# Kernel optimization log

Measured on AMD Instinct MI355X. Metric: run time of the kernel, lower is better.

The kernel has to match this reference:

```python
import jax, jax.numpy as jnp
import numpy as np

B, T, H = 2048, 200, 128
A0, A1 = 64, 16


def setup_inputs() -> dict:
    key = jax.random.key(0)
    ks = jax.random.split(key, 12)
    s = 0.05  # init scale (upstream uses tiny init_std; larger keeps dynamics non-trivial)
    d = {}
    d["query"] = jax.random.normal(ks[0], (B, 1, H), jnp.float32)
    d["keys"] = jax.random.normal(ks[1], (B, T, H), jnp.float32)
    d["W0"] = jax.random.normal(ks[2], (A0, 4 * H), jnp.float32) * s
    d["b0"] = jnp.zeros((A0,), jnp.float32)
    d["W1"] = jax.random.normal(ks[3], (A1, A0), jnp.float32) * s
    d["b1"] = jnp.zeros((A1,), jnp.float32)
    d["Wd"] = jax.random.normal(ks[4], (1, A1), jnp.float32) * s
    d["bd"] = jnp.zeros((1,), jnp.float32)
    d["Wih"] = jax.random.normal(ks[5], (3 * H, H), jnp.float32) * s
    d["Whh"] = jax.random.normal(ks[6], (3 * H, H), jnp.float32) * s
    d["bih"] = jnp.zeros((3 * H,), jnp.float32)
    d["bhh"] = jnp.zeros((3 * H,), jnp.float32)
    d["keys_length"] = jax.random.randint(ks[7], (B, 1), 1, T + 1, jnp.int32)
    return d


def _forward(query, keys, W0, b0, W1, b1, Wd, bd, Wih, Whh, bih, bhh, keys_length):
    b, t, h = keys.shape
    q = jnp.broadcast_to(query, (b, t, h))
    # DIN attention: concat [q, k, q-k, q*k] -> sigmoid MLP -> scalar score
    ai = jnp.concatenate([q, keys, q - keys, q * keys], axis=-1)  # [B,T,4H]
    a = jax.nn.sigmoid(jnp.einsum('bti,oi->bto', ai, W0) + b0)
    a = jax.nn.sigmoid(jnp.einsum('bti,oi->bto', a, W1) + b1)
    score = (jnp.einsum('bti,oi->bto', a, Wd) + bd)[..., 0]  # [B,T]
    valid = jnp.arange(t)[None, :] < keys_length  # [B,T] True at valid steps
    att = jnp.where(valid, score, 0.0)
    # AUGRU over packed (equiv. length-masked) sequence
    gi = jnp.einsum('bti,oi->bto', keys, Wih) + bih  # precomputed input transform [B,T,3H]

    def step(hprev, inp):
        gi_t, a_t, v_t = inp  # [B,3H], [B], [B]
        gh = hprev @ Whh.T + bhh
        i_r, i_z, i_n = jnp.split(gi_t, 3, axis=-1)
        h_r, h_z, h_n = jnp.split(gh, 3, axis=-1)
        r = jax.nn.sigmoid(i_r + h_r)
        z = jax.nn.sigmoid(i_z + h_z)
        n = jnp.tanh(i_n + r * h_n)
        z = a_t[:, None] * z  # attention-modulated update gate
        hnew = (1.0 - z) * hprev + z * n
        hnew = jnp.where(v_t[:, None], hnew, hprev)  # freeze past sequence end
        return hnew, None

    h0 = jnp.zeros((b, h), keys.dtype)
    hT, _ = jax.lax.scan(step, h0, (gi.transpose(1, 0, 2), att.T, valid.T))
    # rows with keys_length == 0 would be zero (here lengths >= 1)
    return hT * (keys_length > 0).astype(hT.dtype)


def reference(query, keys, W0, b0, W1, b1, Wd, bd, Wih, Whh, bih, bhh, keys_length):
    return _forward(query, keys, W0, b0, W1, b1, Wd, bd, Wih, Whh, bih, bhh, keys_length)
```

## Files before the change

### kernel.cpp

```cpp
#include <hip/hip_runtime.h>
#include <stdint.h>
#include <stddef.h>

#define B_N   2048
#define T_SEQ 200
#define H_DIM 128

typedef __attribute__((ext_vector_type(8))) short short8;
typedef __attribute__((ext_vector_type(4))) float floatx4;

#define OFF_ATT 0u
#define OFF_C   819200u
#define OFF_U1  1343488u
#define OFF_FR  1376256u
#define OFF_W1F 1409024u

__device__ __forceinline__ unsigned rnd_bf(float f) {
  union { float f; unsigned u; } v; v.f = f;
  return v.u + 0x7FFFu + ((v.u >> 16) & 1u);
}
__device__ __forceinline__ unsigned short f2bf(float f) {
  return (unsigned short)(rnd_bf(f) >> 16);
}
__device__ __forceinline__ unsigned pack2bf(float lo, float hi) {
  return __builtin_amdgcn_perm(rnd_bf(hi), rnd_bf(lo), 0x07060302u);
}
__device__ __forceinline__ float bf2f(unsigned short u) {
  union { unsigned u; float f; } v; v.u = ((unsigned)u) << 16; return v.f;
}

#define LOG2E 1.4426950408889634f
__device__ __forceinline__ float fsig(float x) {
  return __builtin_amdgcn_rcpf(1.0f + __builtin_amdgcn_exp2f(-LOG2E * x));
}

__device__ __forceinline__ floatx4 mfma16(short8 a, short8 b, floatx4 c) {
  return __builtin_amdgcn_mfma_f32_16x16x32_bf16(a, b, c, 0, 0, 0);
}
__device__ __forceinline__ short8 pack8s(const float* p, float s) {
  short8 r;
#pragma unroll
  for (int j = 0; j < 8; ++j) r[j] = (short)f2bf(p[j] * s);
  return r;
}

__global__ __launch_bounds__(256) void prep_kernel(
    const float* __restrict__ W0, const float* __restrict__ W1,
    float* __restrict__ u1_ws, short8* __restrict__ fr_ws,
    short8* __restrict__ w1f_ws)
{
  const int gid = blockIdx.x * 256 + threadIdx.x;
  const int gs  = gridDim.x * 256;
  for (int i = gid; i < 128 * 64; i += gs) {
    int k = i >> 6, o = i & 63;
    u1_ws[i] = W0[o * 512 + k] + W0[o * 512 + 256 + k];
  }
  for (int f = gid; f < 4 * 8 * 64; f += gs) {
    int ln = f & 63, kc = (f >> 6) & 7, tt = f >> 9;
    int o = tt * 16 + (ln & 15);
    int k0 = kc * 32 + ((ln >> 4) * 8);
    short8 v;
#pragma unroll
    for (int j = 0; j < 8; ++j) {
      int ks = k0 + j;
      float x = (ks < 128) ? (W0[o * 512 + 128 + ks] - W0[o * 512 + 256 + ks])
                           : W0[o * 512 + 384 + (ks - 128)];
      v[j] = (short)f2bf(x);
    }
    fr_ws[f] = v;
  }
  for (int f = gid; f < 2 * 64; f += gs) {
    int ln = f & 63, kc = f >> 6;
    int n = ln & 15, k0 = kc * 32 + ((ln >> 4) * 8);
    short8 v;
#pragma unroll
    for (int j = 0; j < 8; ++j) v[j] = (short)f2bf(W1[n * 64 + k0 + j]);
    w1f_ws[f] = v;
  }
}

__global__ __launch_bounds__(256) void c_kernel(
    const float* __restrict__ query, const float* __restrict__ u1_ws,
    const float* __restrict__ b0, float* __restrict__ c_ws)
{
  const int blk = blockIdx.x, tid = threadIdx.x;
  __shared__ float qs[16 * 128];
  for (int i = tid; i < 512; i += 256)
    *(float4*)&qs[i * 4] = *(const float4*)(query + (size_t)blk * 2048 + i * 4);
  __syncthreads();
  const int o = tid & 63, bb = tid >> 6;
  float a0 = b0[o], a1 = a0, a2 = a0, a3 = a0;
  const float* qr = qs + bb * 512;
#pragma unroll 4
  for (int k = 0; k < 128; ++k) {
    float w = u1_ws[k * 64 + o];
    a0 = fmaf(qr[k], w, a0);
    a1 = fmaf(qr[128 + k], w, a1);
    a2 = fmaf(qr[256 + k], w, a2);
    a3 = fmaf(qr[384 + k], w, a3);
  }
  const int b = blk * 16 + bb * 4;
  c_ws[(b + 0) * 64 + o] = a0;
  c_ws[(b + 1) * 64 + o] = a1;
  c_ws[(b + 2) * 64 + o] = a2;
  c_ws[(b + 3) * 64 + o] = a3;
}

__global__ __launch_bounds__(256) void att_kernel(
    const float* __restrict__ query, const float* __restrict__ keys,
    const float* __restrict__ c_ws, const short8* __restrict__ fr_ws,
    const short8* __restrict__ w1f_ws, const float* __restrict__ b1,
    const float* __restrict__ Wd, const float* __restrict__ bd,
    const int* __restrict__ klen, unsigned short* __restrict__ attb)
{
  const int b   = blockIdx.x;
  const int tid = threadIdx.x;
  const int lane = tid & 63, wv = tid >> 6;
  const int kb = (lane >> 4) * 8;

  __shared__ float qs[H_DIM];
  __shared__ __align__(16) unsigned short A[64][264];
  __shared__ __align__(16) unsigned short a0b[64][72];
  __shared__ float a1s[64][20];

  const int len = klen[b];

  if (tid < H_DIM) qs[tid] = query[(size_t)b * H_DIM + tid];

  short8 bf[8];
  {
    const short8* frp = fr_ws + (size_t)wv * 8 * 64;
#pragma unroll
    for (int kc = 0; kc < 8; ++kc) bf[kc] = frp[kc * 64 + lane];
  }
  short8 w1f0 = w1f_ws[lane], w1f1 = w1f_ws[64 + lane];
  const float b1v = b1[lane & 15];
  const float co = c_ws[(size_t)b * 64 + wv * 16 + (lane & 15)];
  const float bd0 = bd[0];
  float wd_r[16];
#pragma unroll
  for (int i = 0; i < 16; ++i) wd_r[i] = Wd[i];
  __syncthreads();

  int t0 = 0;
  for (; t0 < len; t0 += 64) {
    {
      int tl = tid >> 2, q4 = tid & 3;
      int tg = t0 + tl;
      bool v = (tg < T_SEQ);
      const float* krow = keys + ((size_t)b * T_SEQ + (v ? tg : 0)) * H_DIM + q4 * 32;
#pragma unroll
      for (int i = 0; i < 32; i += 4) {
        float4 kv = v ? *(const float4*)(krow + i) : make_float4(0.f, 0.f, 0.f, 0.f);
        int col = q4 * 32 + i;
        *(unsigned*)&A[tl][col]     = pack2bf(kv.x, kv.y);
        *(unsigned*)&A[tl][col + 2] = pack2bf(kv.z, kv.w);
        *(unsigned*)&A[tl][128 + col]     = pack2bf(kv.x * qs[col + 0], kv.y * qs[col + 1]);
        *(unsigned*)&A[tl][128 + col + 2] = pack2bf(kv.z * qs[col + 2], kv.w * qs[col + 3]);
      }
    }
    __syncthreads();

#pragma unroll
    for (int tt = 0; tt < 4; ++tt) {
      floatx4 acc = {co, co, co, co};
      int row = tt * 16 + (lane & 15);
#pragma unroll
      for (int kc = 0; kc < 8; ++kc)
        acc = mfma16(*(const short8*)&A[row][kc * 32 + kb], bf[kc], acc);
#pragma unroll
      for (int r = 0; r < 4; ++r)
        a0b[tt * 16 + (lane >> 4) * 4 + r][wv * 16 + (lane & 15)] = f2bf(fsig(acc[r]));
    }
    __syncthreads();

    {
      floatx4 acc1 = {b1v, b1v, b1v, b1v};
      int r2 = wv * 16 + (lane & 15);
      acc1 = mfma16(*(const short8*)&a0b[r2][kb],      w1f0, acc1);
      acc1 = mfma16(*(const short8*)&a0b[r2][32 + kb], w1f1, acc1);
#pragma unroll
      for (int r = 0; r < 4; ++r)
        a1s[wv * 16 + (lane >> 4) * 4 + r][lane & 15] = fsig(acc1[r]);
    }
    __syncthreads();

    if (tid < 64) {
      int tg = t0 + tid;
      if (tg < T_SEQ) {
        float s = bd0;
#pragma unroll
        for (int i = 0; i < 16; ++i) s += a1s[tid][i] * wd_r[i];
        attb[(size_t)b * T_SEQ + tg] = (tg < len) ? f2bf(s) : (unsigned short)0;
      }
    }
    __syncthreads();
  }
  for (int i = t0 + tid; i < T_SEQ; i += 256) attb[(size_t)b * T_SEQ + i] = 0;
}

__global__ __launch_bounds__(512, 2) void scan_kernel(
    const float* __restrict__ keys, const float* __restrict__ Wih,
    const float* __restrict__ Whh, const float* __restrict__ bih,
    const float* __restrict__ bhh, const int* __restrict__ klen,
    const unsigned short* __restrict__ attb, float* __restrict__ out)
{
  const int r0 = blockIdx.x * 16;
  const int tid = threadIdx.x;
  const int lane = tid & 63, wv = tid >> 6;

  __shared__ __align__(16) unsigned short hbf[2][16][136];
  __shared__ __align__(16) unsigned short kbf[2][16][136];
  __shared__ __align__(16) float att_s[T_SEQ][16];
  __shared__ int len_s[16];

  if (tid < 16) len_s[tid] = klen[r0 + tid];
  for (int i = tid; i < 16 * 136; i += 512) ((unsigned short*)hbf[0])[i] = 0;
  {
    const unsigned* attw = (const unsigned*)attb;
    for (int i = tid; i < 16 * 100; i += 512) {
      int m = i / 100, t2 = i - m * 100;
      unsigned w = attw[(size_t)(r0 + m) * 100 + t2];
      att_s[2 * t2][m]     = bf2f((unsigned short)(w & 0xFFFFu));
      att_s[2 * t2 + 1][m] = bf2f((unsigned short)(w >> 16));
    }
  }
  const int pm = tid >> 5, pj = (tid & 31) * 4;
  const float* kbase = keys + ((size_t)(r0 + pm) * T_SEQ) * H_DIM + pj;
  {
    float4 k0 = *(const float4*)kbase;
    float4 k1 = *(const float4*)(kbase + H_DIM);
    uint2 p0; p0.x = pack2bf(k0.x, k0.y); p0.y = pack2bf(k0.z, k0.w);
    uint2 p1; p1.x = pack2bf(k1.x, k1.y); p1.y = pack2bf(k1.z, k1.w);
    *(uint2*)&kbf[0][pm][pj] = p0;
    *(uint2*)&kbf[1][pm][pj] = p1;
  }
  float4 kvA = *(const float4*)(kbase + 2 * H_DIM);
  float4 kvB;

  short8 whf[3][4], wif[3][4];
  const int ocol_w = wv * 16 + (lane & 15);
  const int kb = (lane >> 4) * 8;
#pragma unroll
  for (int g = 0; g < 3; ++g) {
    const float sc = (g == 2) ? (-2.0f * LOG2E) : (-LOG2E);
    int row = g * 128 + ocol_w;
#pragma unroll
    for (int kc = 0; kc < 4; ++kc) {
      int kk = kc * 32 + kb;
      whf[g][kc] = pack8s(Whh + (size_t)row * H_DIM + kk, sc);
      wif[g][kc] = pack8s(Wih + (size_t)row * H_DIM + kk, sc);
    }
  }
  const int brow = lane & 15;
  const int oc4  = wv * 16 + (lane >> 4) * 4;
  floatx4 brv, bzv, binv, bhnv;
  {
    floatx4 bi_r = *(const floatx4*)(bih + oc4);
    floatx4 bh_r = *(const floatx4*)(bhh + oc4);
    floatx4 bi_z = *(const floatx4*)(bih + 128 + oc4);
    floatx4 bh_z = *(const floatx4*)(bhh + 128 + oc4);
    floatx4 bi_n = *(const floatx4*)(bih + 256 + oc4);
    floatx4 bh_n = *(const floatx4*)(bhh + 256 + oc4);
#pragma unroll
    for (int r = 0; r < 4; ++r) {
      brv[r]  = -LOG2E * (bi_r[r] + bh_r[r]);
      bzv[r]  = -LOG2E * (bi_z[r] + bh_z[r]);
      binv[r] = -2.0f * LOG2E * bi_n[r];
      bhnv[r] = -2.0f * LOG2E * bh_n[r];
    }
  }

  int tmax = 0;
#pragma unroll
  for (int m = 0; m < 16; ++m) tmax = max(tmax, len_s[m]);
  float hreg[4];
#pragma unroll
  for (int r = 0; r < 4; ++r) hreg[r] = 0.0f;

  __syncthreads();
  floatx4 kAr = brv, kAz = bzv, kAn = binv;
  {
    short8 a0 = *(const short8*)&kbf[0][brow][kb];
    short8 a1 = *(const short8*)&kbf[0][brow][32 + kb];
    short8 a2 = *(const short8*)&kbf[0][brow][64 + kb];
    short8 a3 = *(const short8*)&kbf[0][brow][96 + kb];
    kAr = mfma16(wif[0][0], a0, kAr); kAr = mfma16(wif[0][1], a1, kAr);
    kAr = mfma16(wif[0][2], a2, kAr); kAr = mfma16(wif[0][3], a3, kAr);
    kAz = mfma16(wif[1][0], a0, kAz); kAz = mfma16(wif[1][1], a1, kAz);
    kAz = mfma16(wif[1][2], a2, kAz); kAz = mfma16(wif[1][3], a3, kAz);
    kAn = mfma16(wif[2][0], a0, kAn); kAn = mfma16(wif[2][1], a1, kAn);
    kAn = mfma16(wif[2][2], a2, kAn); kAn = mfma16(wif[2][3], a3, kAn);
  }
  floatx4 kBr, kBz, kBn;
  __syncthreads();

#define SCAN_STEP(BUF, NB, KCr, KCz, KCn, KNr, KNz, KNn, KVC, KVN, TT)          \
  do {                                                                          \
    short8 ah0 = *(const short8*)&hbf[BUF][brow][kb];                           \
    short8 ah1 = *(const short8*)&hbf[BUF][brow][32 + kb];                      \
    short8 ah2 = *(const short8*)&hbf[BUF][brow][64 + kb];                      \
    short8 ah3 = *(const short8*)&hbf[BUF][brow][96 + kb];                      \
    short8 bk0 = *(const short8*)&kbf[NB][brow][kb];                            \
    short8 bk1 = *(const short8*)&kbf[NB][brow][32 + kb];                       \
    short8 bk2 = *(const short8*)&kbf[NB][brow][64 + kb];                       \
    short8 bk3 = *(const short8*)&kbf[NB][brow][96 + kb];                       \
    float att_t = att_s[TT][brow];                                              \
    int tf = (TT) + 3; if (tf > T_SEQ - 1) tf = T_SEQ - 1;                      \
    KVN = *(const float4*)(kbase + (size_t)tf * H_DIM);                         \
    {         \
      uint2 p; p.x = pack2bf(KVC.x, KVC.y); p.y = pack2bf(KVC.z, KVC.w);        \
      *(uint2*)&kbf[BUF][pm][pj] = p;                                           \
    }                                                                           \
        \
    floatx4 arr = KCr, azz = KCz;                                               \
    floatx4 ahn = bhnv;                                                         \
    arr = mfma16(whf[0][0], ah0, arr); arr = mfma16(whf[0][1], ah1, arr);       \
    arr = mfma16(whf[0][2], ah2, arr); arr = mfma16(whf[0][3], ah3, arr);       \
    azz = mfma16(whf[1][0], ah0, azz); azz = mfma16(whf[1][1], ah1, azz);       \
    azz = mfma16(whf[1][2], ah2, azz); azz = mfma16(whf[1][3], ah3, azz);       \
    ahn = mfma16(whf[2][0], ah0, ahn); ahn = mfma16(whf[2][1], ah1, ahn);       \
    ahn = mfma16(whf[2][2], ah2, ahn); ahn = mfma16(whf[2][3], ah3, ahn);       \
                                   \
    KNr = brv; KNz = bzv; KNn = binv;                                           \
    KNr = mfma16(wif[0][0], bk0, KNr); KNr = mfma16(wif[0][1], bk1, KNr);       \
    KNr = mfma16(wif[0][2], bk2, KNr); KNr = mfma16(wif[0][3], bk3, KNr);       \
    KNz = mfma16(wif[1][0], bk0, KNz); KNz = mfma16(wif[1][1], bk1, KNz);       \
    KNz = mfma16(wif[1][2], bk2, KNz); KNz = mfma16(wif[1][3], bk3, KNz);       \
    KNn = mfma16(wif[2][0], bk0, KNn); KNn = mfma16(wif[2][1], bk1, KNn);       \
    KNn = mfma16(wif[2][2], bk2, KNn); KNn = mfma16(wif[2][3], bk3, KNn);       \
    _Pragma("unroll")                                                           \
    for (int r = 0; r < 4; ++r) {                                               \
      float rr = __builtin_amdgcn_rcpf(1.0f + __builtin_amdgcn_exp2f(arr[r]));  \
      float zz = __builtin_amdgcn_rcpf(1.0f + __builtin_amdgcn_exp2f(azz[r]));  \
      float sn = fmaf(rr, ahn[r], KCn[r]);                                      \
      float nn = fmaf(2.0f, __builtin_amdgcn_rcpf(1.0f + __builtin_amdgcn_exp2f(sn)), -1.0f); \
      float z2 = att_t * zz;                                                    \
      hreg[r] = fmaf(z2, nn - hreg[r], hreg[r]);                                \
    }                                                                           \
    {             \
      uint2 hp; hp.x = pack2bf(hreg[0], hreg[1]); hp.y = pack2bf(hreg[2], hreg[3]); \
      *(uint2*)&hbf[NB][brow][oc4] = hp;                                        \
    }                                                                           \
            \
    __asm__ volatile("s_waitcnt lgkmcnt(0)\n\ts_barrier" ::: "memory");         \
  } while (0)

  int t = 0;
  for (; t + 1 < tmax; t += 2) {
    SCAN_STEP(0, 1, kAr, kAz, kAn, kBr, kBz, kBn, kvA, kvB, t);
    SCAN_STEP(1, 0, kBr, kBz, kBn, kAr, kAz, kAn, kvB, kvA, t + 1);
  }
  if (t < tmax) SCAN_STEP(0, 1, kAr, kAz, kAn, kBr, kBz, kBn, kvA, kvB, t);
#undef SCAN_STEP

  {
    float4 o4;
    o4.x = hreg[0]; o4.y = hreg[1]; o4.z = hreg[2]; o4.w = hreg[3];
    *(float4*)&out[(size_t)(r0 + brow) * H_DIM + oc4] = o4;
  }
}

extern "C" void kernel_launch(void* const* d_in, const int* in_sizes, int n_in,
                              void* d_out, int out_size, void* d_ws, size_t ws_size,
                              hipStream_t stream) {
  const float* query = (const float*)d_in[0];
  const float* keys  = (const float*)d_in[1];
  const float* W0    = (const float*)d_in[2];
  const float* b0    = (const float*)d_in[3];
  const float* W1    = (const float*)d_in[4];
  const float* b1    = (const float*)d_in[5];
  const float* Wd    = (const float*)d_in[6];
  const float* bd    = (const float*)d_in[7];
  const float* Wih   = (const float*)d_in[8];
  const float* Whh   = (const float*)d_in[9];
  const float* bih   = (const float*)d_in[10];
  const float* bhh   = (const float*)d_in[11];
  const int*   klen  = (const int*)d_in[12];

  char* ws = (char*)d_ws;
  unsigned short* att_bf = (unsigned short*)(ws + OFF_ATT);
  float*  c_ws  = (float*)(ws + OFF_C);
  float*  u1_ws = (float*)(ws + OFF_U1);
  short8* fr_ws = (short8*)(ws + OFF_FR);
  short8* w1f_ws = (short8*)(ws + OFF_W1F);
  float* out = (float*)d_out;

  hipLaunchKernelGGL(prep_kernel, dim3(8), dim3(256), 0, stream, W0, W1, u1_ws, fr_ws, w1f_ws);
  hipLaunchKernelGGL(c_kernel, dim3(B_N / 16), dim3(256), 0, stream, query, u1_ws, b0, c_ws);
  hipLaunchKernelGGL(att_kernel, dim3(B_N), dim3(256), 0, stream,
                     query, keys, c_ws, fr_ws, w1f_ws, b1, Wd, bd, klen, att_bf);
  hipLaunchKernelGGL(scan_kernel, dim3(B_N / 16), dim3(512), 0, stream,
                     keys, Wih, Whh, bih, bhh, klen, att_bf, out);
}
```

Baseline: 478.3 us.

## Fuse attention MLP into scan kernel with shared-memory union

Folds the per-row attention MLP kernel into the AUGRU scan kernel. Each 512-thread block now computes attention scores for its 16 rows sequentially, writing them straight into shared memory instead of round-tripping a bf16 score buffer through global memory. Shared memory is reused through a union so occupancy is kept. This removes a kernel launch and the global traffic for scores, but the attention work now runs on only 128 blocks, serialised over 16 rows each, instead of 2048 blocks, which may lower parallelism for that phase.

```diff
diff --git a/kernel.cpp b/kernel.cpp
--- a/kernel.cpp
+++ b/kernel.cpp
@@ -106,125 +106,129 @@
   c_ws[(b + 3) * 64 + o] = a3;
 }
 
-__global__ __launch_bounds__(256) void att_kernel(
+struct AttSm {
+  unsigned short A[64][264];
+  unsigned short a0b[64][72];
+  float a1s[64][17];
+  float qs[H_DIM];
+};
+struct ScanSm {
+  unsigned short hbf[2][16][136];
+  unsigned short kbf[2][16][136];
+};
+union SMemU { AttSm att; ScanSm scan; };
+
+__global__ __launch_bounds__(512, 2) void scan_kernel(
     const float* __restrict__ query, const float* __restrict__ keys,
     const float* __restrict__ c_ws, const short8* __restrict__ fr_ws,
     const short8* __restrict__ w1f_ws, const float* __restrict__ b1,
     const float* __restrict__ Wd, const float* __restrict__ bd,
-    const int* __restrict__ klen, unsigned short* __restrict__ attb)
-{
-  const int b   = blockIdx.x;
-  const int tid = threadIdx.x;
-  const int lane = tid & 63, wv = tid >> 6;
-  const int kb = (lane >> 4) * 8;
-
-  __shared__ float qs[H_DIM];
-  __shared__ __align__(16) unsigned short A[64][264];
-  __shared__ __align__(16) unsigned short a0b[64][72];
-  __shared__ float a1s[64][20];
-
-  const int len = klen[b];
-
-  if (tid < H_DIM) qs[tid] = query[(size_t)b * H_DIM + tid];
-
-  short8 bf[8];
-  {
-    const short8* frp = fr_ws + (size_t)wv * 8 * 64;
-#pragma unroll
-    for (int kc = 0; kc < 8; ++kc) bf[kc] = frp[kc * 64 + lane];
-  }
-  short8 w1f0 = w1f_ws[lane], w1f1 = w1f_ws[64 + lane];
-  const float b1v = b1[lane & 15];
-  const float co = c_ws[(size_t)b * 64 + wv * 16 + (lane & 15)];
-  const float bd0 = bd[0];
-  float wd_r[16];
-#pragma unroll
-  for (int i = 0; i < 16; ++i) wd_r[i] = Wd[i];
-  __syncthreads();
-
-  int t0 = 0;
-  for (; t0 < len; t0 += 64) {
-    {
-      int tl = tid >> 2, q4 = tid & 3;
-      int tg = t0 + tl;
-      bool v = (tg < T_SEQ);
-      const float* krow = keys + ((size_t)b * T_SEQ + (v ? tg : 0)) * H_DIM + q4 * 32;
-#pragma unroll
-      for (int i = 0; i < 32; i += 4) {
-        float4 kv = v ? *(const float4*)(krow + i) : make_float4(0.f, 0.f, 0.f, 0.f);
-        int col = q4 * 32 + i;
-        *(unsigned*)&A[tl][col]     = pack2bf(kv.x, kv.y);
-        *(unsigned*)&A[tl][col + 2] = pack2bf(kv.z, kv.w);
-        *(unsigned*)&A[tl][128 + col]     = pack2bf(kv.x * qs[col + 0], kv.y * qs[col + 1]);
-        *(unsigned*)&A[tl][128 + col + 2] = pack2bf(kv.z * qs[col + 2], kv.w * qs[col + 3]);
-      }
-    }
-    __syncthreads();
-
-#pragma unroll
-    for (int tt = 0; tt < 4; ++tt) {
-      floatx4 acc = {co, co, co, co};
-      int row = tt * 16 + (lane & 15);
-#pragma unroll
-      for (int kc = 0; kc < 8; ++kc)
-        acc = mfma16(*(const short8*)&A[row][kc * 32 + kb], bf[kc], acc);
-#pragma unroll
-      for (int r = 0; r < 4; ++r)
-        a0b[tt * 16 + (lane >> 4) * 4 + r][wv * 16 + (lane & 15)] = f2bf(fsig(acc[r]));
-    }
-    __syncthreads();
-
-    {
-      floatx4 acc1 = {b1v, b1v, b1v, b1v};
-      int r2 = wv * 16 + (lane & 15);
-      acc1 = mfma16(*(const short8*)&a0b[r2][kb],      w1f0, acc1);
-      acc1 = mfma16(*(const short8*)&a0b[r2][32 + kb], w1f1, acc1);
-#pragma unroll
-      for (int r = 0; r < 4; ++r)
-        a1s[wv * 16 + (lane >> 4) * 4 + r][lane & 15] = fsig(acc1[r]);
-    }
-    __syncthreads();
-
-    if (tid < 64) {
-      int tg = t0 + tid;
-      if (tg < T_SEQ) {
-        float s = bd0;
-#pragma unroll
-        for (int i = 0; i < 16; ++i) s += a1s[tid][i] * wd_r[i];
-        attb[(size_t)b * T_SEQ + tg] = (tg < len) ? f2bf(s) : (unsigned short)0;
-      }
-    }
-    __syncthreads();
-  }
-  for (int i = t0 + tid; i < T_SEQ; i += 256) attb[(size_t)b * T_SEQ + i] = 0;
-}
-
-__global__ __launch_bounds__(512, 2) void scan_kernel(
-    const float* __restrict__ keys, const float* __restrict__ Wih,
-    const float* __restrict__ Whh, const float* __restrict__ bih,
-    const float* __restrict__ bhh, const int* __restrict__ klen,
-    const unsigned short* __restrict__ attb, float* __restrict__ out)
+    const float* __restrict__ Wih, const float* __restrict__ Whh,
+    const float* __restrict__ bih, const float* __restrict__ bhh,
+    const int* __restrict__ klen, float* __restrict__ out)
 {
   const int r0 = blockIdx.x * 16;
   const int tid = threadIdx.x;
   const int lane = tid & 63, wv = tid >> 6;
-
-  __shared__ __align__(16) unsigned short hbf[2][16][136];
-  __shared__ __align__(16) unsigned short kbf[2][16][136];
+  const int kb = (lane >> 4) * 8;
+
+  __shared__ __align__(16) SMemU sm;
   __shared__ __align__(16) float att_s[T_SEQ][16];
   __shared__ int len_s[16];
 
   if (tid < 16) len_s[tid] = klen[r0 + tid];
-  for (int i = tid; i < 16 * 136; i += 512) ((unsigned short*)hbf[0])[i] = 0;
-  {
-    const unsigned* attw = (const unsigned*)attb;
-    for (int i = tid; i < 16 * 100; i += 512) {
-      int m = i / 100, t2 = i - m * 100;
-      unsigned w = attw[(size_t)(r0 + m) * 100 + t2];
-      att_s[2 * t2][m]     = bf2f((unsigned short)(w & 0xFFFFu));
-      att_s[2 * t2 + 1][m] = bf2f((unsigned short)(w >> 16));
-    }
-  }
+  for (int i = tid; i < T_SEQ * 16; i += 512) ((float*)att_s)[i] = 0.0f;
+  __syncthreads();
+
+  {
+    unsigned short (*A)[264]  = sm.att.A;
+    unsigned short (*a0b)[72] = sm.att.a0b;
+    float (*a1s)[17]          = sm.att.a1s;
+    float* qs                 = sm.att.qs;
+
+    short8 bf[8];
+    {
+      const short8* frp = fr_ws + (size_t)(wv & 3) * 8 * 64;
+#pragma unroll
+      for (int kc = 0; kc < 8; ++kc) bf[kc] = frp[kc * 64 + lane];
+    }
+    short8 w1f0 = w1f_ws[lane], w1f1 = w1f_ws[64 + lane];
+    const float b1v = b1[lane & 15];
+    const float bd0 = bd[0];
+    float wd_r[16];
+#pragma unroll
+    for (int i = 0; i < 16; ++i) wd_r[i] = Wd[i];
+    const int tt0w = (wv >> 2) * 2;
+
+    for (int bb = 0; bb < 16; ++bb) {
+      const int b = r0 + bb;
+      const int len = len_s[bb];
+      if (tid < H_DIM) qs[tid] = query[(size_t)b * H_DIM + tid];
+      const float co = c_ws[(size_t)b * 64 + (wv & 3) * 16 + (lane & 15)];
+      __syncthreads();
+
+      for (int t0 = 0; t0 < len; t0 += 64) {
+        {
+          int tl = tid >> 3, q8 = tid & 7;
+          int tg = t0 + tl;
+          bool v = (tg < T_SEQ);
+          const float* krow = keys + ((size_t)b * T_SEQ + (v ? tg : 0)) * H_DIM + q8 * 16;
+#pragma unroll
+          for (int i = 0; i < 16; i += 4) {
+            float4 kv = v ? *(const float4*)(krow + i) : make_float4(0.f, 0.f, 0.f, 0.f);
+            int col = q8 * 16 + i;
+            *(unsigned*)&A[tl][col]     = pack2bf(kv.x, kv.y);
+            *(unsigned*)&A[tl][col + 2] = pack2bf(kv.z, kv.w);
+            *(unsigned*)&A[tl][128 + col]     = pack2bf(kv.x * qs[col + 0], kv.y * qs[col + 1]);
+            *(unsigned*)&A[tl][128 + col + 2] = pack2bf(kv.z * qs[col + 2], kv.w * qs[col + 3]);
+          }
+        }
+        __syncthreads();
+
+#pragma unroll
+        for (int tt = tt0w; tt < tt0w + 2; ++tt) {
+          floatx4 acc = {co, co, co, co};
+          int row = tt * 16 + (lane & 15);
+#pragma unroll
+          for (int kc = 0; kc < 8; ++kc)
+            acc = mfma16(*(const short8*)&A[row][kc * 32 + kb], bf[kc], acc);
+#pragma unroll
+          for (int r = 0; r < 4; ++r)
+            a0b[tt * 16 + (lane >> 4) * 4 + r][(wv & 3) * 16 + (lane & 15)] =
+                f2bf(fsig(acc[r]));
+        }
+        __syncthreads();
+
+        if (wv < 4) {
+          floatx4 acc1 = {b1v, b1v, b1v, b1v};
+          int r2 = wv * 16 + (lane & 15);
+          acc1 = mfma16(*(const short8*)&a0b[r2][kb],      w1f0, acc1);
+          acc1 = mfma16(*(const short8*)&a0b[r2][32 + kb], w1f1, acc1);
+#pragma unroll
+          for (int r = 0; r < 4; ++r)
+            a1s[wv * 16 + (lane >> 4) * 4 + r][lane & 15] = fsig(acc1[r]);
+        }
+        __syncthreads();
+
+        if (tid < 64) {
+          int tg = t0 + tid;
+          if (tg < len) {
+            float s = bd0;
+#pragma unroll
+            for (int i = 0; i < 16; ++i) s += a1s[tid][i] * wd_r[i];
+            att_s[tg][bb] = s;
+          }
+        }
+        __syncthreads();
+      }
+    }
+  }
+  __syncthreads();
+
+  unsigned short (*hbf)[16][136] = sm.scan.hbf;
+  unsigned short (*kbf)[16][136] = sm.scan.kbf;
+
+  for (int i = tid; i < 16 * 136; i += 512) (&hbf[0][0][0])[i] = 0;
   const int pm = tid >> 5, pj = (tid & 31) * 4;
   const float* kbase = keys + ((size_t)(r0 + pm) * T_SEQ) * H_DIM + pj;
   {
@@ -240,7 +244,6 @@
 
   short8 whf[3][4], wif[3][4];
   const int ocol_w = wv * 16 + (lane & 15);
-  const int kb = (lane >> 4) * 8;
 #pragma unroll
   for (int g = 0; g < 3; ++g) {
     const float sc = (g == 2) ? (-2.0f * LOG2E) : (-LOG2E);
@@ -379,7 +382,6 @@
   const int*   klen  = (const int*)d_in[12];
 
   char* ws = (char*)d_ws;
-  unsigned short* att_bf = (unsigned short*)(ws + OFF_ATT);
   float*  c_ws  = (float*)(ws + OFF_C);
   float*  u1_ws = (float*)(ws + OFF_U1);
   short8* fr_ws = (short8*)(ws + OFF_FR);
@@ -388,8 +390,7 @@
 
   hipLaunchKernelGGL(prep_kernel, dim3(8), dim3(256), 0, stream, W0, W1, u1_ws, fr_ws, w1f_ws);
   hipLaunchKernelGGL(c_kernel, dim3(B_N / 16), dim3(256), 0, stream, query, u1_ws, b0, c_ws);
-  hipLaunchKernelGGL(att_kernel, dim3(B_N), dim3(256), 0, stream,
-                     query, keys, c_ws, fr_ws, w1f_ws, b1, Wd, bd, klen, att_bf);
   hipLaunchKernelGGL(scan_kernel, dim3(B_N / 16), dim3(512), 0, stream,
-                     keys, Wih, Whh, bih, bhh, klen, att_bf, out);
-}
+                     query, keys, c_ws, fr_ws, w1f_ws, b1, Wd, bd,
+                     Wih, Whh, bih, bhh, klen, out);
+}
```

Result: slower. 531.7 us (+11.2%).
